# Performance work log

Measured on AMD Instinct MI355X. Metric: run time of the kernel, lower is better.

The kernel has to match this reference:

```python
import jax, jax.numpy as jnp
import numpy as np

EMBED_DIM = 2048
N_HEADS = 16
N_KV_HEADS = 4
HEAD_DIM = EMBED_DIM // N_HEADS  # 128
NUM_REP = N_HEADS // N_KV_HEADS  # 4
BATCH = 4
SEQLEN = 2048


def setup_inputs() -> dict:
    key = jax.random.key(0)
    kx, kq, kk, kv, ko = jax.random.split(key, 5)
    x = jax.random.normal(kx, (BATCH, SEQLEN, EMBED_DIM), dtype=jnp.float32)
    # Real RoPE table (theta=10000), shape (seqlen, head_dim//2)
    inv_freq = 1.0 / (10000.0 ** (jnp.arange(0, HEAD_DIM, 2, dtype=jnp.float32) / HEAD_DIM))
    t = jnp.arange(SEQLEN, dtype=jnp.float32)
    ang = jnp.outer(t, inv_freq)  # (S, hd/2)
    freqs_cos = jnp.cos(ang)
    freqs_sin = jnp.sin(ang)
    std = 0.02
    wq = jax.random.normal(kq, (EMBED_DIM, N_HEADS * HEAD_DIM), dtype=jnp.float32) * std
    wk = jax.random.normal(kk, (EMBED_DIM, N_KV_HEADS * HEAD_DIM), dtype=jnp.float32) * std
    wv = jax.random.normal(kv, (EMBED_DIM, N_KV_HEADS * HEAD_DIM), dtype=jnp.float32) * std
    wo = jax.random.normal(ko, (N_HEADS * HEAD_DIM, EMBED_DIM), dtype=jnp.float32) * std
    return {"x": x, "freqs_cos": freqs_cos, "freqs_sin": freqs_sin,
            "wq": wq, "wk": wk, "wv": wv, "wo": wo}


def _apply_rope(xh, cos, sin):
    # xh: (b, s, h, hd); cos/sin: (s, hd/2) -> broadcast (1, s, 1, hd/2)
    b, s, h, hd = xh.shape
    xr = xh.reshape(b, s, h, hd // 2, 2)
    x0, x1 = xr[..., 0], xr[..., 1]  # real/imag of complex pairs
    c = cos[None, :, None, :]
    sn = sin[None, :, None, :]
    o0 = x0 * c - x1 * sn
    o1 = x0 * sn + x1 * c
    return jnp.stack([o0, o1], axis=-1).reshape(b, s, h, hd)


def reference(x, freqs_cos, freqs_sin, wq, wk, wv, wo):
    bs, s, _ = x.shape
    xq = (x @ wq).reshape(bs, s, N_HEADS, HEAD_DIM)
    xk = (x @ wk).reshape(bs, s, N_KV_HEADS, HEAD_DIM)
    xv = (x @ wv).reshape(bs, s, N_KV_HEADS, HEAD_DIM)
    xq = _apply_rope(xq, freqs_cos, freqs_sin)
    xk = _apply_rope(xk, freqs_cos, freqs_sin)
    # repeat_kv (GQA): interleave-repeat kv heads to match query heads
    keys = jnp.repeat(xk, NUM_REP, axis=2)    # (b, s, H, hd)
    values = jnp.repeat(xv, NUM_REP, axis=2)
    scale = 1.0 / jnp.sqrt(jnp.float32(HEAD_DIM))
    # SDPA, non-causal
    scores = jnp.einsum('bqhd,bkhd->bhqk', xq, keys) * scale
    probs = jax.nn.softmax(scores, axis=-1)
    out = jnp.einsum('bhqk,bkhd->bqhd', probs, values)
    out = out.reshape(bs, s, N_HEADS * HEAD_DIM)
    return out @ wo
```

## Files before the change

kernel.cpp:

```cpp
#include <hip/hip_runtime.h>
#include <stdint.h>


typedef unsigned short u16;
typedef __bf16 bf16x8 __attribute__((ext_vector_type(8)));
typedef float  f32x4  __attribute__((ext_vector_type(4)));
typedef unsigned int u32x2 __attribute__((ext_vector_type(2)));

#define GLOAD16(gp, lp)                                                        \
  __builtin_amdgcn_global_load_lds(                                            \
      (const __attribute__((address_space(1))) void*)(gp),                     \
      (__attribute__((address_space(3))) void*)(lp), 16, 0, 0)

__device__ __forceinline__ u16 f2b(float f) {
  union { float f; uint32_t u; } v; v.f = f;
  uint32_t r = v.u + 0x7FFFu + ((v.u >> 16) & 1u);
  return (u16)(r >> 16);
}
__device__ __forceinline__ float b2f(u16 h) {
  union { uint32_t u; float f; } v; v.u = ((uint32_t)h) << 16;
  return v.f;
}
__device__ __forceinline__ uint2 pack4(float a, float b, float c, float d) {
  uint2 r;
  asm("v_cvt_pk_bf16_f32 %0, %1, %2" : "=v"(r.x) : "v"(a), "v"(b));
  asm("v_cvt_pk_bf16_f32 %0, %1, %2" : "=v"(r.y) : "v"(c), "v"(d));
  return r;
}

__device__ __forceinline__ void bar_sync() {
  asm volatile("s_waitcnt lgkmcnt(0)" ::: "memory");
  __builtin_amdgcn_s_barrier();
  asm volatile("" ::: "memory");
}

__global__ __launch_bounds__(256) void cast_x_kernel(const float4* __restrict__ in,
                                                     ushort4* __restrict__ out) {
  int i = blockIdx.x * 256 + threadIdx.x;
  float4 v = in[i];
  ushort4 o;
  o.x = f2b(v.x); o.y = f2b(v.y); o.z = f2b(v.z); o.w = f2b(v.w);
  out[i] = o;
}

__global__ __launch_bounds__(256) void wtrans_kernel(const float* __restrict__ W,
                                                     u16* __restrict__ WT,
                                                     int K, int N, float scale) {
  __shared__ float t[32][33];
  int n0 = blockIdx.x * 32, k0 = blockIdx.y * 32;
  int tx = threadIdx.x, ty = threadIdx.y;
  for (int r = 0; r < 4; r++)
    t[ty + r * 8][tx] = W[(size_t)(k0 + ty + r * 8) * N + n0 + tx];
  __syncthreads();
  for (int r = 0; r < 4; r++)
    WT[(size_t)(n0 + ty + r * 8) * K + k0 + tx] = f2b(t[tx][ty + r * 8] * scale);
}

#define KSTEP(CUR, TT)                                                         \
  {                                                                            \
    if ((TT) + 1 < nt) asm volatile("s_waitcnt vmcnt(4)" ::: "memory");        \
    else               asm volatile("s_waitcnt vmcnt(0)" ::: "memory");        \
    bar_sync();                                                                \
    if ((TT) + 2 < nt) {                                                       \
      const size_t k0 = (size_t)((TT) + 2) * 32;                               \
      GLOAD16(Ag + k0, &As[((CUR) + 2) % 3][ldst]);                            \
      GLOAD16(Ag + k0 + (size_t)16 * K, &As[((CUR) + 2) % 3][ldst + 512]);     \
      GLOAD16(Bg + k0, &Bs[((CUR) + 2) % 3][ldst]);                            \
      GLOAD16(Bg + k0 + (size_t)16 * K, &Bs[((CUR) + 2) % 3][ldst + 512]);     \
    }                                                                          \
    bf16x8 af[4], bf[4];                                                       \
    for (int i = 0; i < 4; i++)                                                \
      af[i] = *(const bf16x8*)&As[CUR][wm * 32 + i * 512 + lrd];               \
    for (int i = 0; i < 4; i++)                                                \
      bf[i] = *(const bf16x8*)&Bs[CUR][wn * 32 + i * 512 + lrd];               \
    __builtin_amdgcn_s_setprio(1);                                             \
    for (int mi = 0; mi < 4; mi++)                                             \
      for (int ni = 0; ni < 4; ni++)                                           \
        acc[mi][ni] = __builtin_amdgcn_mfma_f32_16x16x32_bf16(                 \
            af[mi], bf[ni], acc[mi][ni], 0, 0, 0);                             \
    __builtin_amdgcn_s_setprio(0);                                             \
  }

template <bool BF16OUT>
__global__ __launch_bounds__(256) void gemm_bt_kernel(const u16* __restrict__ A,
                                                      const u16* __restrict__ BT,
                                                      void* __restrict__ Cv,
                                                      int K, int N) {
  __shared__ u16 As[3][64 * 64];
  __shared__ u16 Bs[3][64 * 64];
  const int tid = threadIdx.x;
  const int wave = tid >> 6, lane = tid & 63;
  const int quad = lane >> 4, l16 = lane & 15;
  const int wm = (wave >> 1) * 64, wn = (wave & 1) * 64;

  const int nbx = gridDim.x;
  const int nwg = nbx * gridDim.y;
  const int d = blockIdx.x + blockIdx.y * nbx;
  const int w = (d & 7) * (nwg >> 3) + (d >> 3);
  const size_t m0 = (size_t)(w / nbx) * 128, n0 = (size_t)(w % nbx) * 128;

  f32x4 acc[4][4] = {};
  const int srow = wave * 32 + ((lane >> 3) << 1) + ((lane >> 2) & 1);
  const int tcol = ((lane & 3) ^ ((lane >> 3) & 3)) * 8;
  const u16* Ag = A + (m0 + srow) * (size_t)K + tcol;
  const u16* Bg = BT + (n0 + srow) * (size_t)K + tcol;
  const int ldst = wave * 1024;
  const int lrd = (l16 >> 1) * 64 + (l16 & 1) * 32 +
                  ((quad ^ ((l16 >> 1) & 3)) << 3);
  const int nt = K >> 5;

  GLOAD16(Ag, &As[0][ldst]);
  GLOAD16(Ag + (size_t)16 * K, &As[0][ldst + 512]);
  GLOAD16(Bg, &Bs[0][ldst]);
  GLOAD16(Bg + (size_t)16 * K, &Bs[0][ldst + 512]);
  GLOAD16(Ag + 32, &As[1][ldst]);
  GLOAD16(Ag + 32 + (size_t)16 * K, &As[1][ldst + 512]);
  GLOAD16(Bg + 32, &Bs[1][ldst]);
  GLOAD16(Bg + 32 + (size_t)16 * K, &Bs[1][ldst + 512]);

  int t = 0;
  for (; t + 4 < nt; t += 3) {
    KSTEP(0, t);
    KSTEP(1, t + 1);
    KSTEP(2, t + 2);
  }
  KSTEP(0, t);
  KSTEP(1, t + 1);
  KSTEP(2, t + 2);
  KSTEP(0, t + 3);

  for (int mi = 0; mi < 4; mi++)
    for (int ni = 0; ni < 4; ni++)
      for (int r = 0; r < 4; r++) {
        size_t row = m0 + wm + mi * 16 + quad * 4 + r;
        size_t col = n0 + wn + ni * 16 + l16;
        if (BF16OUT) ((u16*)Cv)[row * N + col] = f2b(acc[mi][ni][r]);
        else         ((float*)Cv)[row * N + col] = acc[mi][ni][r];
      }
}

__global__ __launch_bounds__(256) void rope_kernel(u16* __restrict__ QKV,
                                                   const float* __restrict__ cs,
                                                   const float* __restrict__ sn) {
  int tid = blockIdx.x * 256 + threadIdx.x;
  int row = tid / 1280;
  int p = tid - row * 1280;
  int s = row & 2047;
  int head = p >> 6, i = p & 63;
  u16* ptr = QKV + (size_t)row * 3072 + head * 128 + i * 2;
  unsigned int v = *(unsigned int*)ptr;
  float x0 = b2f((u16)(v & 0xffff)), x1 = b2f((u16)(v >> 16));
  float c = cs[s * 64 + i], ss = sn[s * 64 + i];
  u16 o0 = f2b(x0 * c - x1 * ss);
  u16 o1 = f2b(x0 * ss + x1 * c);
  *(unsigned int*)ptr = (unsigned int)o0 | ((unsigned int)o1 << 16);
}

__global__ __launch_bounds__(256) void vtrans_kernel(const u16* __restrict__ QKV,
                                                     u16* __restrict__ Vt) {
  __shared__ u16 t[32][33];
  int b = blockIdx.z >> 2, hk = blockIdx.z & 3;
  int s0 = blockIdx.x * 32, d0 = blockIdx.y * 32;
  int tx = threadIdx.x, ty = threadIdx.y;
  const u16* src = QKV + (size_t)(b * 2048 + s0) * 3072 + 2560 + hk * 128 + d0;
  for (int r = 0; r < 4; r++)
    t[ty + r * 8][tx] = src[(size_t)(ty + r * 8) * 3072 + tx];
  __syncthreads();
  u16* dst = Vt + ((size_t)((b * 4 + hk) * 128 + d0)) * 2048 + s0;
  for (int r = 0; r < 4; r++)
    dst[(size_t)(ty + r * 8) * 2048 + tx] = t[tx][ty + r * 8];
}

__global__ __launch_bounds__(256, 2) void attn_kernel(const u16* __restrict__ QKV,
                                                      const u16* __restrict__ Vt,
                                                      u16* __restrict__ AO) {
  __shared__ u16 KP[128 * 128];
  __shared__ u16 Vls[128 * 128];
  const int tid = threadIdx.x;
  const int wave = tid >> 6, lane = tid & 63;
  const int quad = lane >> 4, l16 = lane & 15;
  const int qt = blockIdx.x, h = blockIdx.y, b = blockIdx.z;
  const int hk = h >> 2;
  const int sw = l16 & 7;

  bf16x8 qf[2][4];
  {
    const u16* Qb = QKV + (size_t)(b * 2048 + qt * 128 + wave * 32) * 3072 + h * 128;
    for (int qb = 0; qb < 2; qb++)
      for (int ki = 0; ki < 4; ki++)
        qf[qb][ki] = *(const bf16x8*)(Qb + (size_t)(qb * 16 + l16) * 3072 + ki * 32 + quad * 8);
  }
  f32x4 o[8][2] = {};
  float m_[2] = {-1e30f, -1e30f}, l_[2] = {0.f, 0.f};

  const u16* Kg0 = QKV + 2048 + hk * 128;
  const u16* Vg0 = Vt + (size_t)((b * 4 + hk) * 128) * 2048;
  const int r4 = lane >> 4, c16 = lane & 15;

  auto stageK = [&](int t) {
    const u16* Kg = Kg0 + (size_t)(b * 2048 + t * 128) * 3072;
    for (int i = 0; i < 8; i++) {
      int grp = i * 4 + wave;
      int row = grp * 4 + r4;
      int ch = c16 ^ (row & 7);
      GLOAD16(Kg + (size_t)row * 3072 + ch * 8, &KP[grp * 512]);
    }
  };
  auto stageV = [&](int t) {
    const u16* Vg = Vg0 + t * 128;
    for (int i = 0; i < 8; i++) {
      int grp = i * 4 + wave;
      int row = grp * 4 + r4;
      int ch = c16 ^ (row & 7);
      GLOAD16(Vg + (size_t)row * 2048 + ch * 8, &Vls[grp * 512]);
    }
  };

  stageK(0);
  stageV(0);
  __syncthreads();

  for (int kt = 0; kt < 16; kt++) {
    if (kt > 0) stageV(kt);

    f32x4 s[8][2];
    for (int kb = 0; kb < 8; kb++) {
      bf16x8 kf[4];
      int a0 = (kb * 16 + l16) * 128 + ((quad ^ sw) << 3);
      for (int ki = 0; ki < 4; ki++)
        kf[ki] = *(const bf16x8*)&KP[a0 ^ (ki * 32)];
      __builtin_amdgcn_s_setprio(1);
      for (int qb = 0; qb < 2; qb++) {
        f32x4 a = {0.f, 0.f, 0.f, 0.f};
        for (int ki = 0; ki < 4; ki++)
          a = __builtin_amdgcn_mfma_f32_16x16x32_bf16(kf[ki], qf[qb][ki], a, 0, 0, 0);
        s[kb][qb] = a;
      }
      __builtin_amdgcn_s_setprio(0);
    }

    bar_sync();
    if (kt < 15) stageK(kt + 1);

    bf16x8 pf[2][4];
    float alch[2];
    for (int qb = 0; qb < 2; qb++) {
      float mk[8];
#pragma unroll
      for (int kb = 0; kb < 8; kb++)
        mk[kb] = fmaxf(fmaxf(s[kb][qb][0], s[kb][qb][1]),
                       fmaxf(s[kb][qb][2], s[kb][qb][3]));
      float mx = fmaxf(fmaxf(fmaxf(mk[0], mk[1]), fmaxf(mk[2], mk[3])),
                       fmaxf(fmaxf(mk[4], mk[5]), fmaxf(mk[6], mk[7])));
      mx = fmaxf(mx, __shfl_xor(mx, 16, 64));
      mx = fmaxf(mx, __shfl_xor(mx, 32, 64));
      float mn = m_[qb], al = 1.0f;
      if (!__all(mx <= m_[qb] + 8.0f)) {
        mn = fmaxf(m_[qb], mx);
        al = exp2f(m_[qb] - mn);
        m_[qb] = mn;
      }
      alch[qb] = al;
      uint2 u[8];
      float rs = 0.f;
#pragma unroll
      for (int kb = 0; kb < 8; kb++) {
        float p0 = exp2f(s[kb][qb][0] - mn), p1 = exp2f(s[kb][qb][1] - mn);
        float p2 = exp2f(s[kb][qb][2] - mn), p3 = exp2f(s[kb][qb][3] - mn);
        u[kb] = pack4(p0, p1, p2, p3);
        rs += (p0 + p1) + (p2 + p3);
      }
      rs += __shfl_xor(rs, 16, 64);
      rs += __shfl_xor(rs, 32, 64);
      l_[qb] = l_[qb] * al + rs;
      const bool qo = (quad & 1) != 0;
#pragma unroll
      for (int ki = 0; ki < 4; ki++) {
        u32x2 r1 = __builtin_amdgcn_permlane32_swap(u[2 * ki].x, u[2 * ki + 1].x, false, false);
        u32x2 r2 = __builtin_amdgcn_permlane32_swap(u[2 * ki].y, u[2 * ki + 1].y, false, false);
        uint32_t t1b = (uint32_t)__shfl_xor((int)r1[1], 16, 64);
        uint32_t t1a = (uint32_t)__shfl_xor((int)r1[0], 16, 64);
        uint32_t t2b = (uint32_t)__shfl_xor((int)r2[1], 16, 64);
        uint32_t t2a = (uint32_t)__shfl_xor((int)r2[0], 16, 64);
        uint4 d;
        d.x = qo ? t1b : (uint32_t)r1[0];
        d.y = qo ? t2b : (uint32_t)r2[0];
        d.z = qo ? (uint32_t)r1[1] : t1a;
        d.w = qo ? (uint32_t)r2[1] : t2a;
        pf[qb][ki] = *(bf16x8*)&d;
      }
    }
    if (alch[0] != 1.0f || alch[1] != 1.0f) {
#pragma unroll
      for (int db = 0; db < 8; db++) {
        o[db][0] *= alch[0];
        o[db][1] *= alch[1];
      }
    }

    if (kt == 15) asm volatile("s_waitcnt vmcnt(0)" ::: "memory");
    else          asm volatile("s_waitcnt vmcnt(8)" ::: "memory");
    bar_sync();

    for (int db = 0; db < 8; db++) {
      bf16x8 vf[4];
      int a0 = (db * 16 + l16) * 128 + ((quad ^ sw) << 3);
      for (int ki = 0; ki < 4; ki++)
        vf[ki] = *(const bf16x8*)&Vls[a0 ^ (ki * 32)];
      __builtin_amdgcn_s_setprio(1);
      for (int qb = 0; qb < 2; qb++)
        for (int ki = 0; ki < 4; ki++)
          o[db][qb] = __builtin_amdgcn_mfma_f32_16x16x32_bf16(vf[ki], pf[qb][ki], o[db][qb], 0, 0, 0);
      __builtin_amdgcn_s_setprio(0);
    }

    asm volatile("s_waitcnt vmcnt(0)" ::: "memory");
    bar_sync();
  }

  float inv[2] = {1.0f / l_[0], 1.0f / l_[1]};
  for (int qb = 0; qb < 2; qb++) {
    int rq = wave * 32 + qb * 16 + l16;
    for (int db = 0; db < 8; db++) {
      int ch = (db * 2 + (quad >> 1)) ^ sw;
      uint2 pv = pack4(o[db][qb][0] * inv[qb], o[db][qb][1] * inv[qb],
                       o[db][qb][2] * inv[qb], o[db][qb][3] * inv[qb]);
      *(uint2*)&KP[rq * 128 + (ch << 3) + (quad & 1) * 4] = pv;
    }
  }
  __syncthreads();
  u16* Ab = AO + (size_t)(b * 2048 + qt * 128) * 2048 + h * 128;
  for (int i = 0; i < 8; i++) {
    int row = i * 16 + (tid >> 4);
    int seg = tid & 15;
    int pc = seg ^ (row & 7);
    *(uint4*)(Ab + (size_t)row * 2048 + seg * 8) = *(const uint4*)&KP[row * 128 + pc * 8];
  }
}

extern "C" void kernel_launch(void* const* d_in, const int* in_sizes, int n_in,
                              void* d_out, int out_size, void* d_ws, size_t ws_size,
                              hipStream_t stream) {
  (void)in_sizes; (void)n_in; (void)out_size; (void)ws_size;
  const float* x    = (const float*)d_in[0];
  const float* fcos = (const float*)d_in[1];
  const float* fsin = (const float*)d_in[2];
  const float* wq   = (const float*)d_in[3];
  const float* wk   = (const float*)d_in[4];
  const float* wv   = (const float*)d_in[5];
  const float* wo   = (const float*)d_in[6];

  char* w = (char*)d_ws;
  u16* xb  = (u16*)w;
  u16* wT  = (u16*)(w + 33554432);
  u16* woT = (u16*)(w + 33554432 + 12582912);
  u16* QKV = (u16*)(w + 33554432 + 12582912 + 8388608);
  u16* Vt  = (u16*)(w + 33554432 + 12582912 + 8388608 + 50331648);
  u16* AO  = xb;

  const float C = 0.08838834764831845f * 1.44269504088896340f;

  cast_x_kernel<<<16384, 256, 0, stream>>>((const float4*)x, (ushort4*)xb);
  wtrans_kernel<<<dim3(64, 64), dim3(32, 8), 0, stream>>>(wq, wT, 2048, 2048, C);
  wtrans_kernel<<<dim3(16, 64), dim3(32, 8), 0, stream>>>(wk, wT + (size_t)2048 * 2048, 2048, 512, 1.0f);
  wtrans_kernel<<<dim3(16, 64), dim3(32, 8), 0, stream>>>(wv, wT + (size_t)2560 * 2048, 2048, 512, 1.0f);
  wtrans_kernel<<<dim3(64, 64), dim3(32, 8), 0, stream>>>(wo, woT, 2048, 2048, 1.0f);

  gemm_bt_kernel<true><<<dim3(24, 64), 256, 0, stream>>>(xb, wT, QKV, 2048, 3072);
  rope_kernel<<<40960, 256, 0, stream>>>(QKV, fcos, fsin);
  vtrans_kernel<<<dim3(64, 4, 16), dim3(32, 8), 0, stream>>>(QKV, Vt);
  attn_kernel<<<dim3(16, 16, 4), 256, 0, stream>>>(QKV, Vt, AO);
  gemm_bt_kernel<false><<<dim3(16, 64), 256, 0, stream>>>(AO, woT, (float*)d_out, 2048, 2048);
}
```

Before: 577.3 us.

## Fuse RoPE and V transpose into QKV GEMM epilogue

The QKV projection GEMM now applies RoPE to Q/K columns in registers, using a lane shuffle to fetch each element's pair partner. For V column tiles it stages the accumulator transposed through shared memory with a rotated layout and writes Vt directly. This removes the separate rope and vtrans kernel launches and their extra global-memory round trips over QKV. The cost is a heavier epilogue that reads cos/sin per element and uses less coalesced bf16 stores for the Q/K part.

```diff
diff --git a/kernel.cpp b/kernel.cpp
--- a/kernel.cpp
+++ b/kernel.cpp
@@ -63,16 +63,16 @@
     bar_sync();                                                                \
     if ((TT) + 2 < nt) {                                                       \
       const size_t k0 = (size_t)((TT) + 2) * 32;                               \
-      GLOAD16(Ag + k0, &As[((CUR) + 2) % 3][ldst]);                            \
-      GLOAD16(Ag + k0 + (size_t)16 * K, &As[((CUR) + 2) % 3][ldst + 512]);     \
-      GLOAD16(Bg + k0, &Bs[((CUR) + 2) % 3][ldst]);                            \
-      GLOAD16(Bg + k0 + (size_t)16 * K, &Bs[((CUR) + 2) % 3][ldst + 512]);     \
+      GLOAD16(Ag + k0, &SH[((CUR) + 2) % 3 * 4096 + ldst]);                    \
+      GLOAD16(Ag + k0 + (size_t)16 * K, &SH[((CUR) + 2) % 3 * 4096 + ldst + 512]); \
+      GLOAD16(Bg + k0, &SH[12288 + ((CUR) + 2) % 3 * 4096 + ldst]);            \
+      GLOAD16(Bg + k0 + (size_t)16 * K, &SH[12288 + ((CUR) + 2) % 3 * 4096 + ldst + 512]); \
     }                                                                          \
     bf16x8 af[4], bf[4];                                                       \
     for (int i = 0; i < 4; i++)                                                \
-      af[i] = *(const bf16x8*)&As[CUR][wm * 32 + i * 512 + lrd];               \
+      af[i] = *(const bf16x8*)&SH[(CUR) * 4096 + wm * 32 + i * 512 + lrd];     \
     for (int i = 0; i < 4; i++)                                                \
-      bf[i] = *(const bf16x8*)&Bs[CUR][wn * 32 + i * 512 + lrd];               \
+      bf[i] = *(const bf16x8*)&SH[12288 + (CUR) * 4096 + wn * 32 + i * 512 + lrd]; \
     __builtin_amdgcn_s_setprio(1);                                             \
     for (int mi = 0; mi < 4; mi++)                                             \
       for (int ni = 0; ni < 4; ni++)                                           \
@@ -85,9 +85,11 @@
 __global__ __launch_bounds__(256) void gemm_bt_kernel(const u16* __restrict__ A,
                                                       const u16* __restrict__ BT,
                                                       void* __restrict__ Cv,
-                                                      int K, int N) {
-  __shared__ u16 As[3][64 * 64];
-  __shared__ u16 Bs[3][64 * 64];
+                                                      int K, int N,
+                                                      const float* __restrict__ cs,
+                                                      const float* __restrict__ sn,
+                                                      u16* __restrict__ Vt) {
+  __shared__ u16 SH[24576];
   const int tid = threadIdx.x;
   const int wave = tid >> 6, lane = tid & 63;
   const int quad = lane >> 4, l16 = lane & 15;
@@ -109,14 +111,14 @@
                   ((quad ^ ((l16 >> 1) & 3)) << 3);
   const int nt = K >> 5;
 
-  GLOAD16(Ag, &As[0][ldst]);
-  GLOAD16(Ag + (size_t)16 * K, &As[0][ldst + 512]);
-  GLOAD16(Bg, &Bs[0][ldst]);
-  GLOAD16(Bg + (size_t)16 * K, &Bs[0][ldst + 512]);
-  GLOAD16(Ag + 32, &As[1][ldst]);
-  GLOAD16(Ag + 32 + (size_t)16 * K, &As[1][ldst + 512]);
-  GLOAD16(Bg + 32, &Bs[1][ldst]);
-  GLOAD16(Bg + 32 + (size_t)16 * K, &Bs[1][ldst + 512]);
+  GLOAD16(Ag, &SH[ldst]);
+  GLOAD16(Ag + (size_t)16 * K, &SH[ldst + 512]);
+  GLOAD16(Bg, &SH[12288 + ldst]);
+  GLOAD16(Bg + (size_t)16 * K, &SH[12288 + ldst + 512]);
+  GLOAD16(Ag + 32, &SH[4096 + ldst]);
+  GLOAD16(Ag + 32 + (size_t)16 * K, &SH[4096 + ldst + 512]);
+  GLOAD16(Bg + 32, &SH[12288 + 4096 + ldst]);
+  GLOAD16(Bg + 32 + (size_t)16 * K, &SH[12288 + 4096 + ldst + 512]);
 
   int t = 0;
   for (; t + 4 < nt; t += 3) {
@@ -129,46 +131,56 @@
   KSTEP(2, t + 2);
   KSTEP(0, t + 3);
 
-  for (int mi = 0; mi < 4; mi++)
-    for (int ni = 0; ni < 4; ni++)
-      for (int r = 0; r < 4; r++) {
-        size_t row = m0 + wm + mi * 16 + quad * 4 + r;
-        size_t col = n0 + wn + ni * 16 + l16;
-        if (BF16OUT) ((u16*)Cv)[row * N + col] = f2b(acc[mi][ni][r]);
-        else         ((float*)Cv)[row * N + col] = acc[mi][ni][r];
-      }
-}
-
-__global__ __launch_bounds__(256) void rope_kernel(u16* __restrict__ QKV,
-                                                   const float* __restrict__ cs,
-                                                   const float* __restrict__ sn) {
-  int tid = blockIdx.x * 256 + threadIdx.x;
-  int row = tid / 1280;
-  int p = tid - row * 1280;
-  int s = row & 2047;
-  int head = p >> 6, i = p & 63;
-  u16* ptr = QKV + (size_t)row * 3072 + head * 128 + i * 2;
-  unsigned int v = *(unsigned int*)ptr;
-  float x0 = b2f((u16)(v & 0xffff)), x1 = b2f((u16)(v >> 16));
-  float c = cs[s * 64 + i], ss = sn[s * 64 + i];
-  u16 o0 = f2b(x0 * c - x1 * ss);
-  u16 o1 = f2b(x0 * ss + x1 * c);
-  *(unsigned int*)ptr = (unsigned int)o0 | ((unsigned int)o1 << 16);
-}
-
-__global__ __launch_bounds__(256) void vtrans_kernel(const u16* __restrict__ QKV,
-                                                     u16* __restrict__ Vt) {
-  __shared__ u16 t[32][33];
-  int b = blockIdx.z >> 2, hk = blockIdx.z & 3;
-  int s0 = blockIdx.x * 32, d0 = blockIdx.y * 32;
-  int tx = threadIdx.x, ty = threadIdx.y;
-  const u16* src = QKV + (size_t)(b * 2048 + s0) * 3072 + 2560 + hk * 128 + d0;
-  for (int r = 0; r < 4; r++)
-    t[ty + r * 8][tx] = src[(size_t)(ty + r * 8) * 3072 + tx];
-  __syncthreads();
-  u16* dst = Vt + ((size_t)((b * 4 + hk) * 128 + d0)) * 2048 + s0;
-  for (int r = 0; r < 4; r++)
-    dst[(size_t)(ty + r * 8) * 2048 + tx] = t[tx][ty + r * 8];
+  if constexpr (BF16OUT) {
+    if (n0 >= 2560) {
+      bar_sync();
+      for (int mi = 0; mi < 4; mi++)
+        for (int ni = 0; ni < 4; ni++) {
+          int dl = wn + ni * 16 + l16;
+          int sl = wm + mi * 16 + quad * 4;
+          uint2 pv = pack4(acc[mi][ni][0], acc[mi][ni][1],
+                           acc[mi][ni][2], acc[mi][ni][3]);
+          int rot = 8 * (dl & 15);
+          *(uint32_t*)&SH[dl * 128 + ((sl + rot) & 127)] = pv.x;
+          *(uint32_t*)&SH[dl * 128 + ((sl + 2 + rot) & 127)] = pv.y;
+        }
+      __syncthreads();
+      const int bb = (int)(m0 >> 11), s0v = (int)(m0 & 2047);
+      const int hk = (int)((n0 - 2560) >> 7);
+      u16* dst0 = Vt + ((size_t)(bb * 4 + hk) * 128) * 2048 + s0v;
+      for (int i = 0; i < 8; i++) {
+        int dd = i * 16 + (tid >> 4);
+        int seg = tid & 15;
+        int src = dd * 128 + ((seg + (dd & 15)) & 15) * 8;
+        *(uint4*)(dst0 + (size_t)dd * 2048 + seg * 8) = *(const uint4*)&SH[src];
+      }
+    } else {
+      for (int mi = 0; mi < 4; mi++)
+        for (int ni = 0; ni < 4; ni++) {
+          int col = (int)n0 + wn + ni * 16 + l16;
+          int ii = (col & 127) >> 1;
+          bool odd = (col & 1) != 0;
+          for (int r = 0; r < 4; r++) {
+            int row = (int)m0 + wm + mi * 16 + quad * 4 + r;
+            int s = row & 2047;
+            float v = acc[mi][ni][r];
+            float pv = __shfl_xor(v, 1, 64);
+            float c_ = cs[(size_t)s * 64 + ii];
+            float s_ = sn[(size_t)s * 64 + ii];
+            float out = odd ? (pv * s_ + v * c_) : (v * c_ - pv * s_);
+            ((u16*)Cv)[(size_t)row * N + col] = f2b(out);
+          }
+        }
+    }
+  } else {
+    for (int mi = 0; mi < 4; mi++)
+      for (int ni = 0; ni < 4; ni++)
+        for (int r = 0; r < 4; r++) {
+          size_t row = m0 + wm + mi * 16 + quad * 4 + r;
+          size_t col = n0 + wn + ni * 16 + l16;
+          ((float*)Cv)[row * N + col] = acc[mi][ni][r];
+        }
+  }
 }
 
 __global__ __launch_bounds__(256, 2) void attn_kernel(const u16* __restrict__ QKV,
@@ -366,9 +378,9 @@
   wtrans_kernel<<<dim3(16, 64), dim3(32, 8), 0, stream>>>(wv, wT + (size_t)2560 * 2048, 2048, 512, 1.0f);
   wtrans_kernel<<<dim3(64, 64), dim3(32, 8), 0, stream>>>(wo, woT, 2048, 2048, 1.0f);
 
-  gemm_bt_kernel<true><<<dim3(24, 64), 256, 0, stream>>>(xb, wT, QKV, 2048, 3072);
-  rope_kernel<<<40960, 256, 0, stream>>>(QKV, fcos, fsin);
-  vtrans_kernel<<<dim3(64, 4, 16), dim3(32, 8), 0, stream>>>(QKV, Vt);
+  gemm_bt_kernel<true><<<dim3(24, 64), 256, 0, stream>>>(xb, wT, QKV, 2048, 3072,
+                                                         fcos, fsin, Vt);
   attn_kernel<<<dim3(16, 16, 4), 256, 0, stream>>>(QKV, Vt, AO);
-  gemm_bt_kernel<false><<<dim3(16, 64), 256, 0, stream>>>(AO, woT, (float*)d_out, 2048, 2048);
-}
+  gemm_bt_kernel<false><<<dim3(16, 64), 256, 0, stream>>>(AO, woT, (float*)d_out, 2048, 2048,
+                                                          nullptr, nullptr, nullptr);
+}
```

Result: faster. 545.8 us (-5.5%).
